# Performance work log

Hardware: AMD Instinct MI355X
Metric: run time of the kernel (lower is better)

Reference implementation:

```python
import jax, jax.numpy as jnp
import numpy as np

GAMMA = 0.99
GAE_LAMBDA = 0.95
CLIP = 0.2
ENT_COEF = 0.01
VF_COEF = 0.5


def setup_inputs() -> dict:
    key = jax.random.key(0)
    ks = jax.random.split(key, 12)
    T, D, H, A = 65536, 512, 256, 16
    obs = jax.random.normal(ks[0], (T, D), dtype=jnp.float32)
    actions = jax.random.randint(ks[1], (T,), 0, A, dtype=jnp.int32)
    logprobs = jax.random.normal(ks[2], (T,), dtype=jnp.float32)
    rewards = jax.random.normal(ks[3], (T,), dtype=jnp.float32)
    terms = jax.random.uniform(ks[4], (T,), dtype=jnp.float32)
    values = jax.random.normal(ks[5], (T,), dtype=jnp.float32)
    # orthogonal-init-like scaling (std sqrt(2) for trunk, 0.01 actor, 1.0 critic)
    W1 = jax.random.normal(ks[6], (D, H), dtype=jnp.float32) * np.float32(np.sqrt(2.0 / D))
    b1 = jnp.zeros((H,), jnp.float32)
    W2 = jax.random.normal(ks[7], (H, H), dtype=jnp.float32) * np.float32(np.sqrt(2.0 / H))
    b2 = jnp.zeros((H,), jnp.float32)
    Wa = jax.random.normal(ks[8], (H, A), dtype=jnp.float32) * np.float32(0.01 / np.sqrt(H))
    ba = jnp.zeros((A,), jnp.float32)
    Wc = jax.random.normal(ks[9], (H, 1), dtype=jnp.float32) * np.float32(1.0 / np.sqrt(H))
    bc = jnp.zeros((1,), jnp.float32)
    return {"obs": obs, "actions": actions, "logprobs": logprobs, "rewards": rewards,
            "terms": terms, "values": values, "W1": W1, "b1": b1, "W2": W2, "b2": b2,
            "Wa": Wa, "ba": ba, "Wc": Wc, "bc": bc}


def reference(obs, actions, logprobs, rewards, terms, values,
              W1, b1, W2, b2, Wa, ba, Wc, bc):
    # ---- GAE (torch.no_grad in original -> stop_gradient) ----
    nonterm = 1.0 - terms                                   # [T]
    next_vals = jnp.concatenate([values[1:], jnp.zeros((1,), values.dtype)])
    delta = rewards + GAMMA * next_vals * nonterm - values  # [T]

    def step(carry, x):  # reverse recurrence a_t = d_t + g*l*nt_t * a_{t+1}
        d, nt = x
        g = d + GAMMA * GAE_LAMBDA * nt * carry
        return g, g

    _, adv = jax.lax.scan(step, jnp.float32(0.0), (delta, nonterm), reverse=True)
    adv = jax.lax.stop_gradient(adv)
    returns = adv + jax.lax.stop_gradient(values)
    vals_old = jax.lax.stop_gradient(values)

    # ---- actor-critic MLP (get_action_and_value) ----
    hidden = jnp.tanh(jnp.tanh(obs @ W1 + b1) @ W2 + b2)    # [T,256]
    logits = hidden @ Wa + ba                               # [T,A]
    logp = jax.nn.log_softmax(logits, axis=-1)
    newlp = jnp.take_along_axis(logp, actions[:, None].astype(jnp.int32), axis=1)[:, 0]
    entropy = -jnp.sum(jnp.exp(logp) * logp, axis=-1)       # [T]
    value = (hidden @ Wc + bc)[:, 0]                        # [T]

    # ---- clipped PPO losses (single full-batch minibatch) ----
    ratio = jnp.exp(newlp - logprobs)
    a = (adv - adv.mean()) / (adv.std() + 1e-8)
    pg_loss = jnp.maximum(-a * ratio, -a * jnp.clip(ratio, 1.0 - CLIP, 1.0 + CLIP)).mean()
    v_clipped = vals_old + jnp.clip(value - vals_old, -CLIP, CLIP)
    v_loss = 0.5 * jnp.maximum((value - returns) ** 2, (v_clipped - returns) ** 2).mean()
    loss = pg_loss - ENT_COEF * entropy.mean() + VF_COEF * v_loss
    return loss
```

## Files before the change

### kernel.cpp

```cpp
#include <hip/hip_runtime.h>


#define TT 65536

typedef float f32x4 __attribute__((ext_vector_type(4)));
typedef __bf16 bf16x8 __attribute__((ext_vector_type(8)));
typedef unsigned short u16x8 __attribute__((ext_vector_type(8)));
typedef unsigned short u16x4 __attribute__((ext_vector_type(4)));

__device__ __forceinline__ unsigned short f2bf(float f) {
    unsigned int u = __float_as_uint(f);
    unsigned int r = (u + 0x7fffu + ((u >> 16) & 1u)) >> 16;
    return (unsigned short)r;
}

__device__ __forceinline__ float fast_tanh(float x) {
    float e = __expf(2.0f * x);
    return fmaf(-2.0f, __builtin_amdgcn_rcpf(e + 1.0f), 1.0f);
}

__device__ __forceinline__ void suffix_scan256(float* sC, float* sD, int i) {
    float c = sC[i], d = sD[i];
#pragma unroll
    for (int s = 1; s < 256; s <<= 1) {
        float c2 = 1.0f, d2 = 0.0f;
        if (i + s < 256) { c2 = sC[i + s]; d2 = sD[i + s]; }
        __syncthreads();
        d = d + c * d2;
        c = c * c2;
        sC[i] = c; sD[i] = d;
        __syncthreads();
    }
}

__device__ __forceinline__ void gae_cd(const float* rewards, const float* terms,
                                       const float* values, int t, float* c, float* d) {
    float nt = 1.0f - terms[t];
    float nv = (t + 1 < TT) ? values[t + 1] : 0.0f;
    *d = rewards[t] + 0.99f * nv * nt - values[t];
    *c = 0.99f * 0.95f * nt;
}

__global__ void k_prep_gae1(const float* __restrict__ W1, const float* __restrict__ W2,
                            const float* __restrict__ Wa, const float* __restrict__ Wc,
                            unsigned short* __restrict__ W1T, unsigned short* __restrict__ W2T,
                            unsigned short* __restrict__ WavT,
                            const float* __restrict__ rewards, const float* __restrict__ terms,
                            const float* __restrict__ values, float* __restrict__ aggC,
                            float* __restrict__ aggD) {
    if (blockIdx.x < 800) {
        int idx = blockIdx.x * 256 + threadIdx.x;
        if (idx < 131072) {
            int n = idx >> 9, k = idx & 511;
            W1T[idx] = f2bf(W1[k * 256 + n]);
        } else if (idx < 196608) {
            int i = idx - 131072;
            int n = i >> 8, k = i & 255;
            W2T[i] = f2bf(W2[k * 256 + n]);
        } else if (idx < 204800) {
            int i = idx - 196608;
            int r = i >> 8, k = i & 255;
            float v = (r < 16) ? Wa[k * 16 + r] : ((r == 16) ? Wc[k] : 0.0f);
            WavT[i] = f2bf(v);
        }
        return;
    }
    __shared__ float sC[256], sD[256];
    int i = threadIdx.x;
    int b = blockIdx.x - 800;
    int t = b * 256 + i;
    float c, d;
    gae_cd(rewards, terms, values, t, &c, &d);
    sC[i] = c; sD[i] = d;
    __syncthreads();
    suffix_scan256(sC, sD, i);
    if (i == 0) { aggC[b] = sC[0]; aggD[b] = sD[0]; }
}

__global__ void k_gae3(const float* __restrict__ rewards, const float* __restrict__ terms,
                       const float* __restrict__ values, const float* __restrict__ aggC,
                       const float* __restrict__ aggD, float* __restrict__ adv,
                       float* __restrict__ ret, float* __restrict__ sumP) {
    __shared__ float sC[256], sD[256];
    int i = threadIdx.x, b = blockIdx.x;
    sC[i] = aggC[i]; sD[i] = aggD[i];
    __syncthreads();
    suffix_scan256(sC, sD, i);
    float carry = (b < 255) ? sD[b + 1] : 0.0f;
    __syncthreads();

    int t = b * 256 + i;
    float c, d;
    gae_cd(rewards, terms, values, t, &c, &d);
    sC[i] = c; sD[i] = d;
    __syncthreads();
    suffix_scan256(sC, sD, i);
    float a = sD[i] + sC[i] * carry;
    adv[t] = a;
    ret[t] = a + values[t];
    __syncthreads();
    sC[i] = a; sD[i] = a * a;
    __syncthreads();
#pragma unroll
    for (int s = 128; s > 0; s >>= 1) {
        if (i < s) { sC[i] += sC[i + s]; sD[i] += sD[i + s]; }
        __syncthreads();
    }
    if (i == 0) { sumP[2 * b] = sC[0]; sumP[2 * b + 1] = sD[0]; }
}

__global__ __launch_bounds__(1024, 4) void k_mlp(
    const float* __restrict__ obs, const int* __restrict__ actions,
    const float* __restrict__ logprobs, const float* __restrict__ values,
    const float* __restrict__ b1, const float* __restrict__ b2,
    const float* __restrict__ ba, const float* __restrict__ bc,
    const unsigned short* __restrict__ W1T, const unsigned short* __restrict__ W2T,
    const unsigned short* __restrict__ WavT, const float* __restrict__ adv,
    const float* __restrict__ ret, const float* __restrict__ sumP,
    float* __restrict__ lossP) {
    __shared__ __align__(16) unsigned short smA[2][128 * 32];
    __shared__ __align__(16) unsigned short smB[2][256 * 32];
    __shared__ __align__(16) unsigned short smH[128 * 256];
    __shared__ float red2[16];
    float* red = (float*)smH;

    const int tid = threadIdx.x;
    const int wid = tid >> 6;
    const int lane = tid & 63;
    const int cl = lane & 15;
    const int gg = lane >> 4;
    const int mw = wid >> 2;
    const int nw = wid & 3;
    const int bm0 = blockIdx.x * 128;

    const int arow = tid >> 3;
    const int acol = (tid & 7) * 4;
    const int adst = arow * 32 +
        ((((acol >> 3) ^ ((arow >> 1) & 3)) << 3) | (acol & 4));
    const float* aSrc = obs + (size_t)(bm0 + arow) * 512 + acol;

    const int brow = tid >> 2;
    const int bslot = tid & 3;
    const int bdst = brow * 32 + ((bslot ^ ((brow >> 1) & 3)) << 3);
    const unsigned short* b1Src = W1T + (size_t)brow * 512 + bslot * 8;
    const unsigned short* b2Src = W2T + (size_t)brow * 256 + bslot * 8;
    const int wrow = tid >> 5;
    const int we = (tid & 31) * 8;
    const int wdst = wrow * 256 + (we ^ ((wrow & 7) << 3));

    float4 areg = *(const float4*)aSrc;
    u16x8 breg = *(const u16x8*)b1Src;

    float meanA, rstdA;
    {
        if (tid < 256) { red[tid] = sumP[2 * tid]; red[256 + tid] = sumP[2 * tid + 1]; }
        __syncthreads();
#pragma unroll
        for (int s = 128; s > 0; s >>= 1) {
            if (tid < s) { red[tid] += red[tid + s]; red[256 + tid] += red[256 + tid + s]; }
            __syncthreads();
        }
        meanA = red[0] * (1.0f / TT);
        float var = red[256] * (1.0f / TT) - meanA * meanA;
        rstdA = 1.0f / (sqrtf(fmaxf(var, 0.0f)) + 1e-8f);
        __syncthreads();
    }

    float b1v[4], b2v[4];
#pragma unroll
    for (int n = 0; n < 4; ++n) {
        int c = nw * 64 + n * 16 + cl;
        b1v[n] = b1[c];
        b2v[n] = b2[c];
    }
    const float bav = ba[cl];
    const float bc0 = bc[0];

    f32x4 acc[2][4];
#pragma unroll
    for (int m = 0; m < 2; ++m)
#pragma unroll
        for (int n = 0; n < 4; ++n) acc[m][n] = (f32x4){0.f, 0.f, 0.f, 0.f};

    auto writeA = [&](int buf) {
        u16x4 ac;
        ac[0] = f2bf(areg.x); ac[1] = f2bf(areg.y);
        ac[2] = f2bf(areg.z); ac[3] = f2bf(areg.w);
        *(u16x4*)&smA[buf][adst] = ac;
    };

    writeA(0);
    *(u16x8*)&smB[0][bdst] = breg;
    __syncthreads();

#pragma unroll
    for (int t = 0; t < 16; ++t) {
        if (t < 15) {
            areg = *(const float4*)(aSrc + (t + 1) * 32);
            breg = *(const u16x8*)(b1Src + (t + 1) * 32);
        } else {
            breg = *(const u16x8*)b2Src;
        }
        bf16x8 av[2], bv[4];
#pragma unroll
        for (int m = 0; m < 2; ++m) {
            int ra = mw * 32 + m * 16 + cl;
            av[m] = *(const bf16x8*)&smA[t & 1][ra * 32 + ((gg ^ ((ra >> 1) & 3)) << 3)];
        }
#pragma unroll
        for (int n = 0; n < 4; ++n) {
            int rb = nw * 64 + n * 16 + cl;
            bv[n] = *(const bf16x8*)&smB[t & 1][rb * 32 + ((gg ^ ((rb >> 1) & 3)) << 3)];
        }
#pragma unroll
        for (int m = 0; m < 2; ++m)
#pragma unroll
            for (int n = 0; n < 4; ++n)
                acc[m][n] = __builtin_amdgcn_mfma_f32_16x16x32_bf16(av[m], bv[n], acc[m][n], 0, 0, 0);
        if (t < 15) writeA((t + 1) & 1);
        *(u16x8*)&smB[(t + 1) & 1][bdst] = breg;
        __syncthreads();
    }

#pragma unroll
    for (int m = 0; m < 2; ++m)
#pragma unroll
        for (int n = 0; n < 4; ++n)
#pragma unroll
            for (int j = 0; j < 4; ++j) {
                int r = mw * 32 + m * 16 + gg * 4 + j;
                int c = nw * 64 + n * 16 + cl;
                smH[r * 256 + (c ^ ((r & 7) << 3))] = f2bf(fast_tanh(acc[m][n][j] + b1v[n]));
                acc[m][n][j] = 0.0f;
            }
    __syncthreads();

#pragma unroll
    for (int t = 0; t < 8; ++t) {
        if (t < 7) breg = *(const u16x8*)(b2Src + (t + 1) * 32);
        else       breg = *(const u16x8*)(WavT + wrow * 256 + we);
        bf16x8 av[2], bv[4];
#pragma unroll
        for (int m = 0; m < 2; ++m) {
            int ra = mw * 32 + m * 16 + cl;
            av[m] = *(const bf16x8*)&smH[ra * 256 + ((t * 32 + gg * 8) ^ ((ra & 7) << 3))];
        }
#pragma unroll
        for (int n = 0; n < 4; ++n) {
            int rb = nw * 64 + n * 16 + cl;
            bv[n] = *(const bf16x8*)&smB[t & 1][rb * 32 + ((gg ^ ((rb >> 1) & 3)) << 3)];
        }
#pragma unroll
        for (int m = 0; m < 2; ++m)
#pragma unroll
            for (int n = 0; n < 4; ++n)
                acc[m][n] = __builtin_amdgcn_mfma_f32_16x16x32_bf16(av[m], bv[n], acc[m][n], 0, 0, 0);
        if (t < 7) *(u16x8*)&smB[(t + 1) & 1][bdst] = breg;
        else       *(u16x8*)&smB[0][wdst] = breg;
        __syncthreads();
    }

#pragma unroll
    for (int m = 0; m < 2; ++m)
#pragma unroll
        for (int n = 0; n < 4; ++n)
#pragma unroll
            for (int j = 0; j < 4; ++j) {
                int r = mw * 32 + m * 16 + gg * 4 + j;
                int c = nw * 64 + n * 16 + cl;
                smH[r * 256 + (c ^ ((r & 7) << 3))] = f2bf(fast_tanh(acc[m][n][j] + b2v[n]));
            }
    __syncthreads();

    float lsum = 0.0f;
    if (wid < 8) {
        f32x4 acc_a = {0.f, 0.f, 0.f, 0.f}, acc_v = {0.f, 0.f, 0.f, 0.f};
#pragma unroll
        for (int kk = 0; kk < 8; ++kk) {
            int r = wid * 16 + cl;
            bf16x8 av = *(const bf16x8*)&smH[r * 256 + ((kk * 32 + gg * 8) ^ ((r & 7) << 3))];
            int ra2 = cl;
            bf16x8 bva = *(const bf16x8*)&smB[0][ra2 * 256 + ((kk * 32 + gg * 8) ^ ((ra2 & 7) << 3))];
            int rv = 16 + cl;
            bf16x8 bvv = *(const bf16x8*)&smB[0][rv * 256 + ((kk * 32 + gg * 8) ^ ((rv & 7) << 3))];
            acc_a = __builtin_amdgcn_mfma_f32_16x16x32_bf16(av, bva, acc_a, 0, 0, 0);
            acc_v = __builtin_amdgcn_mfma_f32_16x16x32_bf16(av, bvv, acc_v, 0, 0, 0);
        }

        const int t0 = bm0 + wid * 16;
#pragma unroll
        for (int j = 0; j < 4; ++j) {
            int t = t0 + gg * 4 + j;
            float lg = acc_a[j] + bav;
            float mx = lg;
#pragma unroll
            for (int dd = 1; dd < 16; dd <<= 1) mx = fmaxf(mx, __shfl_xor(mx, dd));
            float ex = __expf(lg - mx);
            float se = ex;
#pragma unroll
            for (int dd = 1; dd < 16; dd <<= 1) se += __shfl_xor(se, dd);
            float ls = __logf(se);
            float lp = lg - mx - ls;
            float pl = __expf(lp) * lp;
            float ent = pl;
#pragma unroll
            for (int dd = 1; dd < 16; dd <<= 1) ent += __shfl_xor(ent, dd);
            ent = -ent;
            int act = actions[t];
            float newlp = __shfl(lp, (lane & 48) | act);
            float val = __shfl(acc_v[j], lane & 48) + bc0;

            float lpo = logprobs[t];
            float at = (adv[t] - meanA) * rstdA;
            float rt = ret[t];
            float vo = values[t];
            float ratio = __expf(newlp - lpo);
            float rcl = fminf(fmaxf(ratio, 0.8f), 1.2f);
            float pg = fmaxf(-at * ratio, -at * rcl);
            float vcl = vo + fminf(fmaxf(val - vo, -0.2f), 0.2f);
            float dv = val - rt, dvc = vcl - rt;
            float vl = fmaxf(dv * dv, dvc * dvc);
            if (cl == 0) lsum += pg - 0.01f * ent + 0.25f * vl;
        }
        lsum += __shfl_xor(lsum, 16);
        lsum += __shfl_xor(lsum, 32);
    }
    if (wid < 8 && lane == 0) red2[wid] = lsum;
    __syncthreads();
    if (tid == 0) {
        float s = 0.0f;
#pragma unroll
        for (int w = 0; w < 8; ++w) s += red2[w];
        lossP[blockIdx.x] = s;
    }
}

__global__ void k_final(const float* __restrict__ lossP, float* __restrict__ out) {
    __shared__ float s[256];
    int i = threadIdx.x;
    s[i] = lossP[i] + lossP[i + 256];
    __syncthreads();
#pragma unroll
    for (int st = 128; st > 0; st >>= 1) {
        if (i < st) s[i] += s[i + st];
        __syncthreads();
    }
    if (i == 0) out[0] = s[0] * (1.0f / TT);
}

extern "C" void kernel_launch(void* const* d_in, const int* in_sizes, int n_in,
                              void* d_out, int out_size, void* d_ws, size_t ws_size,
                              hipStream_t stream) {
    const float* obs      = (const float*)d_in[0];
    const int*   actions  = (const int*)d_in[1];
    const float* logprobs = (const float*)d_in[2];
    const float* rewards  = (const float*)d_in[3];
    const float* terms    = (const float*)d_in[4];
    const float* values   = (const float*)d_in[5];
    const float* W1 = (const float*)d_in[6];
    const float* b1 = (const float*)d_in[7];
    const float* W2 = (const float*)d_in[8];
    const float* b2 = (const float*)d_in[9];
    const float* Wa = (const float*)d_in[10];
    const float* ba = (const float*)d_in[11];
    const float* Wc = (const float*)d_in[12];
    const float* bc = (const float*)d_in[13];

    char* ws = (char*)d_ws;
    unsigned short* W1T  = (unsigned short*)(ws + 0);
    unsigned short* W2T  = (unsigned short*)(ws + 262144);
    unsigned short* WavT = (unsigned short*)(ws + 393216);
    float* advp  = (float*)(ws + 409600);
    float* retp  = (float*)(ws + 671744);
    float* aggC  = (float*)(ws + 933888);
    float* aggD  = (float*)(ws + 934912);
    float* sumP  = (float*)(ws + 936960);
    float* lossP = (float*)(ws + 939072);

    k_prep_gae1<<<1056, 256, 0, stream>>>(W1, W2, Wa, Wc, W1T, W2T, WavT,
                                          rewards, terms, values, aggC, aggD);
    k_gae3<<<256, 256, 0, stream>>>(rewards, terms, values, aggC, aggD, advp, retp, sumP);
    k_mlp<<<512, 1024, 0, stream>>>(obs, actions, logprobs, values, b1, b2, ba, bc,
                                    W1T, W2T, WavT, advp, retp, sumP, lossP);
    k_final<<<1, 256, 0, stream>>>(lossP, (float*)d_out);
}
```

Baseline: 73.31 us.

## Stream pre-swizzled weights into LDS asynchronously with smaller 64-row MLP blocks

The prep kernel now writes the bf16 weight matrices already in the swizzled LDS tile order, so k_mlp can copy each weight tile straight from global memory into LDS with global_load_lds instead of staging it through registers. k_mlp shrinks from 128 rows and 1024 threads to 64 rows and 512 threads per block. Each wave now owns a 32-column strip across all 64 rows, and the grid doubles to 1024 blocks, so k_final sums four partials per thread. The intent is to free registers, overlap weight fetches with MFMA work and raise occupancy, at the cost of each weight being re-read by twice as many blocks.

```diff
diff --git a/kernel.cpp b/kernel.cpp
--- a/kernel.cpp
+++ b/kernel.cpp
@@ -17,6 +17,12 @@
 __device__ __forceinline__ float fast_tanh(float x) {
     float e = __expf(2.0f * x);
     return fmaf(-2.0f, __builtin_amdgcn_rcpf(e + 1.0f), 1.0f);
+}
+
+__device__ __forceinline__ void async_lds16(void* lds, const void* g) {
+    __builtin_amdgcn_global_load_lds(
+        (const __attribute__((address_space(1))) unsigned int*)g,
+        (__attribute__((address_space(3))) unsigned int*)lds, 16, 0, 0);
 }
 
 __device__ __forceinline__ void suffix_scan256(float* sC, float* sD, int i) {
@@ -51,16 +57,24 @@
     if (blockIdx.x < 800) {
         int idx = blockIdx.x * 256 + threadIdx.x;
         if (idx < 131072) {
-            int n = idx >> 9, k = idx & 511;
-            W1T[idx] = f2bf(W1[k * 256 + n]);
+            int kt = idx >> 13;
+            int L = (idx & 8191) >> 3, e = idx & 7;
+            int row = L >> 2, p = L & 3;
+            int k = kt * 32 + (((p ^ ((row >> 1) & 3)) << 3) | e);
+            W1T[idx] = f2bf(W1[k * 256 + row]);
         } else if (idx < 196608) {
             int i = idx - 131072;
-            int n = i >> 8, k = i & 255;
-            W2T[i] = f2bf(W2[k * 256 + n]);
+            int kt = i >> 13;
+            int L = (i & 8191) >> 3, e = i & 7;
+            int row = L >> 2, p = L & 3;
+            int k = kt * 32 + (((p ^ ((row >> 1) & 3)) << 3) | e);
+            W2T[i] = f2bf(W2[k * 256 + row]);
         } else if (idx < 204800) {
             int i = idx - 196608;
-            int r = i >> 8, k = i & 255;
-            float v = (r < 16) ? Wa[k * 16 + r] : ((r == 16) ? Wc[k] : 0.0f);
+            int L = i >> 3, e = i & 7;
+            int row = L >> 5, ec = (L & 31) << 3;
+            int k = ((ec ^ ((row & 7) << 3)) | e);
+            float v = (row < 16) ? Wa[k * 16 + row] : ((row == 16) ? Wc[k] : 0.0f);
             WavT[i] = f2bf(v);
         }
         return;
@@ -109,7 +123,7 @@
     if (i == 0) { sumP[2 * b] = sC[0]; sumP[2 * b + 1] = sD[0]; }
 }
 
-__global__ __launch_bounds__(1024, 4) void k_mlp(
+__global__ __launch_bounds__(512, 4) void k_mlp(
     const float* __restrict__ obs, const int* __restrict__ actions,
     const float* __restrict__ logprobs, const float* __restrict__ values,
     const float* __restrict__ b1, const float* __restrict__ b2,
@@ -118,20 +132,19 @@
     const unsigned short* __restrict__ WavT, const float* __restrict__ adv,
     const float* __restrict__ ret, const float* __restrict__ sumP,
     float* __restrict__ lossP) {
-    __shared__ __align__(16) unsigned short smA[2][128 * 32];
-    __shared__ __align__(16) unsigned short smB[2][256 * 32];
-    __shared__ __align__(16) unsigned short smH[128 * 256];
-    __shared__ float red2[16];
-    float* red = (float*)smH;
+    __shared__ __align__(16) unsigned char SM[73728];
+    unsigned short* smB = (unsigned short*)SM;
+    unsigned short* smA = (unsigned short*)(SM + 32768);
+    unsigned short* smH = (unsigned short*)(SM + 40960);
+    float* red = (float*)(SM + 40960);
+    float* red2 = (float*)(SM + 32768);
 
     const int tid = threadIdx.x;
     const int wid = tid >> 6;
     const int lane = tid & 63;
     const int cl = lane & 15;
     const int gg = lane >> 4;
-    const int mw = wid >> 2;
-    const int nw = wid & 3;
-    const int bm0 = blockIdx.x * 128;
+    const int bm0 = blockIdx.x * 64;
 
     const int arow = tid >> 3;
     const int acol = (tid & 7) * 4;
@@ -139,17 +152,12 @@
         ((((acol >> 3) ^ ((arow >> 1) & 3)) << 3) | (acol & 4));
     const float* aSrc = obs + (size_t)(bm0 + arow) * 512 + acol;
 
-    const int brow = tid >> 2;
-    const int bslot = tid & 3;
-    const int bdst = brow * 32 + ((bslot ^ ((brow >> 1) & 3)) << 3);
-    const unsigned short* b1Src = W1T + (size_t)brow * 512 + bslot * 8;
-    const unsigned short* b2Src = W2T + (size_t)brow * 256 + bslot * 8;
-    const int wrow = tid >> 5;
-    const int we = (tid & 31) * 8;
-    const int wdst = wrow * 256 + (we ^ ((wrow & 7) << 3));
-
     float4 areg = *(const float4*)aSrc;
-    u16x8 breg = *(const u16x8*)b1Src;
+#pragma unroll
+    for (int c = 0; c < 2; ++c) {
+        int chunk = wid * 2 + c;
+        async_lds16(&smB[chunk * 512], W1T + chunk * 512 + lane * 8);
+    }
 
     float meanA, rstdA;
     {
@@ -166,70 +174,70 @@
         __syncthreads();
     }
 
-    float b1v[4], b2v[4];
-#pragma unroll
-    for (int n = 0; n < 4; ++n) {
-        int c = nw * 64 + n * 16 + cl;
+    float b1v[2], b2v[2];
+#pragma unroll
+    for (int n = 0; n < 2; ++n) {
+        int c = wid * 32 + n * 16 + cl;
         b1v[n] = b1[c];
         b2v[n] = b2[c];
     }
     const float bav = ba[cl];
     const float bc0 = bc[0];
 
-    f32x4 acc[2][4];
-#pragma unroll
-    for (int m = 0; m < 2; ++m)
-#pragma unroll
-        for (int n = 0; n < 4; ++n) acc[m][n] = (f32x4){0.f, 0.f, 0.f, 0.f};
+    f32x4 acc[4][2];
+#pragma unroll
+    for (int m = 0; m < 4; ++m)
+#pragma unroll
+        for (int n = 0; n < 2; ++n) acc[m][n] = (f32x4){0.f, 0.f, 0.f, 0.f};
 
     auto writeA = [&](int buf) {
         u16x4 ac;
         ac[0] = f2bf(areg.x); ac[1] = f2bf(areg.y);
         ac[2] = f2bf(areg.z); ac[3] = f2bf(areg.w);
-        *(u16x4*)&smA[buf][adst] = ac;
+        *(u16x4*)&smA[buf * 2048 + adst] = ac;
     };
 
     writeA(0);
-    *(u16x8*)&smB[0][bdst] = breg;
     __syncthreads();
 
 #pragma unroll
     for (int t = 0; t < 16; ++t) {
-        if (t < 15) {
-            areg = *(const float4*)(aSrc + (t + 1) * 32);
-            breg = *(const u16x8*)(b1Src + (t + 1) * 32);
-        } else {
-            breg = *(const u16x8*)b2Src;
-        }
-        bf16x8 av[2], bv[4];
-#pragma unroll
-        for (int m = 0; m < 2; ++m) {
-            int ra = mw * 32 + m * 16 + cl;
-            av[m] = *(const bf16x8*)&smA[t & 1][ra * 32 + ((gg ^ ((ra >> 1) & 3)) << 3)];
-        }
-#pragma unroll
-        for (int n = 0; n < 4; ++n) {
-            int rb = nw * 64 + n * 16 + cl;
-            bv[n] = *(const bf16x8*)&smB[t & 1][rb * 32 + ((gg ^ ((rb >> 1) & 3)) << 3)];
-        }
-#pragma unroll
-        for (int m = 0; m < 2; ++m)
-#pragma unroll
-            for (int n = 0; n < 4; ++n)
+        const unsigned short* bsrc = (t < 15) ? (W1T + (t + 1) * 8192) : W2T;
+#pragma unroll
+        for (int c = 0; c < 2; ++c) {
+            int chunk = wid * 2 + c;
+            async_lds16(&smB[((t + 1) & 1) * 8192 + chunk * 512], bsrc + chunk * 512 + lane * 8);
+        }
+        if (t < 15) areg = *(const float4*)(aSrc + (t + 1) * 32);
+
+        bf16x8 av[4], bv[2];
+#pragma unroll
+        for (int m = 0; m < 4; ++m) {
+            int ra = m * 16 + cl;
+            av[m] = *(const bf16x8*)&smA[(t & 1) * 2048 + ra * 32 + ((gg ^ ((ra >> 1) & 3)) << 3)];
+        }
+#pragma unroll
+        for (int n = 0; n < 2; ++n) {
+            int rb = wid * 32 + n * 16 + cl;
+            bv[n] = *(const bf16x8*)&smB[(t & 1) * 8192 + rb * 32 + ((gg ^ ((rb >> 1) & 3)) << 3)];
+        }
+#pragma unroll
+        for (int m = 0; m < 4; ++m)
+#pragma unroll
+            for (int n = 0; n < 2; ++n)
                 acc[m][n] = __builtin_amdgcn_mfma_f32_16x16x32_bf16(av[m], bv[n], acc[m][n], 0, 0, 0);
         if (t < 15) writeA((t + 1) & 1);
-        *(u16x8*)&smB[(t + 1) & 1][bdst] = breg;
-        __syncthreads();
-    }
-
-#pragma unroll
-    for (int m = 0; m < 2; ++m)
-#pragma unroll
-        for (int n = 0; n < 4; ++n)
+        __syncthreads();
+    }
+
+#pragma unroll
+    for (int m = 0; m < 4; ++m)
+#pragma unroll
+        for (int n = 0; n < 2; ++n)
 #pragma unroll
             for (int j = 0; j < 4; ++j) {
-                int r = mw * 32 + m * 16 + gg * 4 + j;
-                int c = nw * 64 + n * 16 + cl;
+                int r = m * 16 + gg * 4 + j;
+                int c = wid * 32 + n * 16 + cl;
                 smH[r * 256 + (c ^ ((r & 7) << 3))] = f2bf(fast_tanh(acc[m][n][j] + b1v[n]));
                 acc[m][n][j] = 0.0f;
             }
@@ -237,52 +245,54 @@
 
 #pragma unroll
     for (int t = 0; t < 8; ++t) {
-        if (t < 7) breg = *(const u16x8*)(b2Src + (t + 1) * 32);
-        else       breg = *(const u16x8*)(WavT + wrow * 256 + we);
-        bf16x8 av[2], bv[4];
-#pragma unroll
-        for (int m = 0; m < 2; ++m) {
-            int ra = mw * 32 + m * 16 + cl;
+        const unsigned short* bsrc = (t < 7) ? (W2T + (t + 1) * 8192) : WavT;
+#pragma unroll
+        for (int c = 0; c < 2; ++c) {
+            int chunk = wid * 2 + c;
+            async_lds16(&smB[((t + 1) & 1) * 8192 + chunk * 512], bsrc + chunk * 512 + lane * 8);
+        }
+        bf16x8 av[4], bv[2];
+#pragma unroll
+        for (int m = 0; m < 4; ++m) {
+            int ra = m * 16 + cl;
             av[m] = *(const bf16x8*)&smH[ra * 256 + ((t * 32 + gg * 8) ^ ((ra & 7) << 3))];
         }
 #pragma unroll
-        for (int n = 0; n < 4; ++n) {
-            int rb = nw * 64 + n * 16 + cl;
-            bv[n] = *(const bf16x8*)&smB[t & 1][rb * 32 + ((gg ^ ((rb >> 1) & 3)) << 3)];
-        }
-#pragma unroll
-        for (int m = 0; m < 2; ++m)
-#pragma unroll
-            for (int n = 0; n < 4; ++n)
+        for (int n = 0; n < 2; ++n) {
+            int rb = wid * 32 + n * 16 + cl;
+            bv[n] = *(const bf16x8*)&smB[(t & 1) * 8192 + rb * 32 + ((gg ^ ((rb >> 1) & 3)) << 3)];
+        }
+#pragma unroll
+        for (int m = 0; m < 4; ++m)
+#pragma unroll
+            for (int n = 0; n < 2; ++n)
                 acc[m][n] = __builtin_amdgcn_mfma_f32_16x16x32_bf16(av[m], bv[n], acc[m][n], 0, 0, 0);
-        if (t < 7) *(u16x8*)&smB[(t + 1) & 1][bdst] = breg;
-        else       *(u16x8*)&smB[0][wdst] = breg;
-        __syncthreads();
-    }
-
-#pragma unroll
-    for (int m = 0; m < 2; ++m)
-#pragma unroll
-        for (int n = 0; n < 4; ++n)
+        __syncthreads();
+    }
+
+#pragma unroll
+    for (int m = 0; m < 4; ++m)
+#pragma unroll
+        for (int n = 0; n < 2; ++n)
 #pragma unroll
             for (int j = 0; j < 4; ++j) {
-                int r = mw * 32 + m * 16 + gg * 4 + j;
-                int c = nw * 64 + n * 16 + cl;
+                int r = m * 16 + gg * 4 + j;
+                int c = wid * 32 + n * 16 + cl;
                 smH[r * 256 + (c ^ ((r & 7) << 3))] = f2bf(fast_tanh(acc[m][n][j] + b2v[n]));
             }
     __syncthreads();
 
     float lsum = 0.0f;
-    if (wid < 8) {
+    if (wid < 4) {
         f32x4 acc_a = {0.f, 0.f, 0.f, 0.f}, acc_v = {0.f, 0.f, 0.f, 0.f};
 #pragma unroll
         for (int kk = 0; kk < 8; ++kk) {
             int r = wid * 16 + cl;
             bf16x8 av = *(const bf16x8*)&smH[r * 256 + ((kk * 32 + gg * 8) ^ ((r & 7) << 3))];
             int ra2 = cl;
-            bf16x8 bva = *(const bf16x8*)&smB[0][ra2 * 256 + ((kk * 32 + gg * 8) ^ ((ra2 & 7) << 3))];
+            bf16x8 bva = *(const bf16x8*)&smB[ra2 * 256 + ((kk * 32 + gg * 8) ^ ((ra2 & 7) << 3))];
             int rv = 16 + cl;
-            bf16x8 bvv = *(const bf16x8*)&smB[0][rv * 256 + ((kk * 32 + gg * 8) ^ ((rv & 7) << 3))];
+            bf16x8 bvv = *(const bf16x8*)&smB[rv * 256 + ((kk * 32 + gg * 8) ^ ((rv & 7) << 3))];
             acc_a = __builtin_amdgcn_mfma_f32_16x16x32_bf16(av, bva, acc_a, 0, 0, 0);
             acc_v = __builtin_amdgcn_mfma_f32_16x16x32_bf16(av, bvv, acc_v, 0, 0, 0);
         }
@@ -325,20 +335,16 @@
         lsum += __shfl_xor(lsum, 16);
         lsum += __shfl_xor(lsum, 32);
     }
-    if (wid < 8 && lane == 0) red2[wid] = lsum;
-    __syncthreads();
-    if (tid == 0) {
-        float s = 0.0f;
-#pragma unroll
-        for (int w = 0; w < 8; ++w) s += red2[w];
-        lossP[blockIdx.x] = s;
-    }
+    __syncthreads();
+    if (wid < 4 && lane == 0) red2[wid] = lsum;
+    __syncthreads();
+    if (tid == 0) lossP[blockIdx.x] = red2[0] + red2[1] + red2[2] + red2[3];
 }
 
 __global__ void k_final(const float* __restrict__ lossP, float* __restrict__ out) {
     __shared__ float s[256];
     int i = threadIdx.x;
-    s[i] = lossP[i] + lossP[i + 256];
+    s[i] = lossP[i] + lossP[i + 256] + lossP[i + 512] + lossP[i + 768];
     __syncthreads();
 #pragma unroll
     for (int st = 128; st > 0; st >>= 1) {
@@ -380,7 +386,7 @@
     k_prep_gae1<<<1056, 256, 0, stream>>>(W1, W2, Wa, Wc, W1T, W2T, WavT,
                                           rewards, terms, values, aggC, aggD);
     k_gae3<<<256, 256, 0, stream>>>(rewards, terms, values, aggC, aggD, advp, retp, sumP);
-    k_mlp<<<512, 1024, 0, stream>>>(obs, actions, logprobs, values, b1, b2, ba, bc,
+    k_mlp<<<1024, 512, 0, stream>>>(obs, actions, logprobs, values, b1, b2, ba, bc,
                                     W1T, W2T, WavT, advp, retp, sumP, lossP);
     k_final<<<1, 256, 0, stream>>>(lossP, (float*)d_out);
 }
```

New measurement: 65.90 us. -10.1%, faster.
